# Kernel optimization log

Measured on AMD Instinct MI355X. Metric: run time of the kernel, lower is better.

The kernel has to match this reference:

```python
import jax, jax.numpy as jnp
import numpy as np

DIM = 1024
HEADS = 16
DIM_HEAD = 64
INNER = HEADS * DIM_HEAD  # 1024
EPS = 1e-5


def _layernorm(x, gamma, beta):
    mu = jnp.mean(x, axis=-1, keepdims=True)
    var = jnp.var(x, axis=-1, keepdims=True)
    return (x - mu) * jax.lax.rsqrt(var + EPS) * gamma + beta


def setup_inputs() -> dict:
    key = jax.random.key(0)
    ks = jax.random.split(key, 7)
    b, m, n = 8, 4096, 64
    x = jax.random.normal(ks[0], (b, m, DIM), dtype=jnp.float32)
    latents = jax.random.normal(ks[1], (b, n, DIM), dtype=jnp.float32)
    # LayerNorm params (torch default: weight=1, bias=0; randomize slightly)
    g1 = jnp.ones((DIM,), jnp.float32)
    b1 = jnp.zeros((DIM,), jnp.float32)
    g2 = jnp.ones((DIM,), jnp.float32)
    b2 = jnp.zeros((DIM,), jnp.float32)
    s = 1.0 / np.sqrt(DIM)
    Wq = jax.random.normal(ks[2], (DIM, INNER), jnp.float32) * s   # [in, out]
    Wkv = jax.random.normal(ks[3], (DIM, 2 * INNER), jnp.float32) * s
    Wo = jax.random.normal(ks[4], (INNER, DIM), jnp.float32) * s
    return {"x": x, "latents": latents, "g1": g1, "b1": b1,
            "g2": g2, "b2": b2, "Wq": Wq, "Wkv": Wkv, "Wo": Wo}


def reference(x, latents, g1, b1, g2, b2, Wq, Wkv, Wo):
    b, n, _ = latents.shape
    h, d = HEADS, DIM_HEAD
    scale = d ** -0.5

    xn = _layernorm(x, g1, b1)
    ln = _layernorm(latents, g2, b2)

    q = ln @ Wq                              # [b, n, inner]
    kv_input = jnp.concatenate((xn, ln), axis=1)  # [b, m+n, dim]
    kv = kv_input @ Wkv                      # [b, m+n, 2*inner]
    k, v = jnp.split(kv, 2, axis=-1)
    s_kv = kv_input.shape[1]

    q = q.reshape(b, n, h, d).transpose(0, 2, 1, 3)      # bhnd
    k = k.reshape(b, s_kv, h, d).transpose(0, 2, 1, 3)   # bhsd
    v = v.reshape(b, s_kv, h, d).transpose(0, 2, 1, 3)   # bhsd

    # double-scaling trick: (q*scale) @ (k*scale)^T  => effective 1/d
    weight = jnp.einsum('bhnd,bhsd->bhns', q * scale, k * scale)
    weight = jax.nn.softmax(weight.astype(jnp.float32), axis=-1).astype(weight.dtype)
    out = jnp.einsum('bhns,bhsd->bhnd', weight, v)
    out = out.transpose(0, 2, 1, 3).reshape(b, n, h * d)
    return out @ Wo
```

## Files before the change

### kernel.cpp

```cpp
#include <hip/hip_runtime.h>

typedef __bf16 bf16;
typedef bf16 bf16x4_t __attribute__((ext_vector_type(4)));
typedef bf16 bf16x8_t __attribute__((ext_vector_type(8)));
typedef float f32x4_t __attribute__((ext_vector_type(4)));

#define DI __device__ __forceinline__

DI void gload_lds16(const void* g, void* l) {
  __builtin_amdgcn_global_load_lds((const __attribute__((address_space(1))) void*)g,
                                   (__attribute__((address_space(3))) void*)l, 16, 0, 0);
}

DI f32x4_t mfma16(bf16x8_t a, bf16x8_t b, f32x4_t c) {
  return __builtin_amdgcn_mfma_f32_16x16x32_bf16(a, b, c, 0, 0, 0);
}

DI unsigned short bfbits(float f) {
  bf16 h = (bf16)f;
  return __builtin_bit_cast(unsigned short, h);
}

__global__ __launch_bounds__(256) void ln_all(const float* __restrict__ x,
                                              const float* __restrict__ lat,
                                              const float* __restrict__ g1,
                                              const float* __restrict__ b1,
                                              const float* __restrict__ g2,
                                              const float* __restrict__ b2,
                                              bf16* __restrict__ kv_in,
                                              bf16* __restrict__ lnq) {
  const int row = blockIdx.x;
  const int t = threadIdx.x;
  const float* in;
  const float* gamma;
  const float* beta;
  size_t orow;
  bool dual;
  int lrow = 0;
  if (row < 32768) {
    in = x + (size_t)row * 1024;
    gamma = g1; beta = b1;
    const int b = row >> 12, r2 = row & 4095;
    orow = (size_t)b * 4160 + r2;
    dual = false;
  } else {
    const int r = row - 32768;
    in = lat + (size_t)r * 1024;
    gamma = g2; beta = b2;
    const int b = r >> 6, r2 = r & 63;
    orow = (size_t)b * 4160 + 4096 + r2;
    dual = true;
    lrow = r;
  }
  const float4 v = ((const float4*)in)[t];
  float s = v.x + v.y + v.z + v.w;
  float q = v.x * v.x + v.y * v.y + v.z * v.z + v.w * v.w;
#pragma unroll
  for (int off = 1; off < 64; off <<= 1) {
    s += __shfl_xor(s, off);
    q += __shfl_xor(q, off);
  }
  __shared__ float red[8];
  const int w = t >> 6;
  if ((t & 63) == 0) { red[w] = s; red[w + 4] = q; }
  __syncthreads();
  s = red[0] + red[1] + red[2] + red[3];
  q = red[4] + red[5] + red[6] + red[7];
  const float mu = s * (1.f / 1024.f);
  const float var = q * (1.f / 1024.f) - mu * mu;
  const float rs = rsqrtf(var + 1e-5f);
  const float4 gv = ((const float4*)gamma)[t];
  const float4 bv = ((const float4*)beta)[t];
  bf16x4_t o;
  o[0] = (bf16)((v.x - mu) * rs * gv.x + bv.x);
  o[1] = (bf16)((v.y - mu) * rs * gv.y + bv.y);
  o[2] = (bf16)((v.z - mu) * rs * gv.z + bv.z);
  o[3] = (bf16)((v.w - mu) * rs * gv.w + bv.w);
  *(bf16x4_t*)(kv_in + orow * 1024 + t * 4) = o;
  if (dual) {
    *(bf16x4_t*)(lnq + (size_t)lrow * 1024 + t * 4) = o;
  }
}

__global__ __launch_bounds__(256) void transpose_all(const float* __restrict__ Wq,
                                                     const float* __restrict__ Wkv,
                                                     const float* __restrict__ Wo,
                                                     bf16* __restrict__ Wq_t,
                                                     bf16* __restrict__ Wkv_t,
                                                     bf16* __restrict__ Wo_t) {
  __shared__ float tile[32][33];
  const int bid = blockIdx.x;
  const float* W;
  bf16* Wt;
  int C, t0;
  if (bid < 1024)      { W = Wq;  Wt = Wq_t;  C = 1024; t0 = bid; }
  else if (bid < 3072) { W = Wkv; Wt = Wkv_t; C = 2048; t0 = bid - 1024; }
  else                 { W = Wo;  Wt = Wo_t;  C = 1024; t0 = bid - 3072; }
  const int R = 1024;
  const int ntx = C >> 5;
  const int c0 = (t0 % ntx) * 32, r0 = (t0 / ntx) * 32;
  const int tx = threadIdx.x, ty = threadIdx.y;
#pragma unroll
  for (int j = 0; j < 4; ++j)
    tile[ty + j * 8][tx] = W[(size_t)(r0 + ty + j * 8) * C + c0 + tx];
  __syncthreads();
#pragma unroll
  for (int j = 0; j < 4; ++j)
    Wt[(size_t)(c0 + ty + j * 8) * R + r0 + tx] = (bf16)tile[tx][ty + j * 8];
}

__global__ __launch_bounds__(256) void gemm_bt(const bf16* __restrict__ A,
                                               const bf16* __restrict__ Bt,
                                               float* __restrict__ Cf,
                                               int M, int N, int K) {
  __shared__ bf16 As[128 * 32];
  __shared__ bf16 Bs[128 * 32];
  const int tid = threadIdx.x;
  const int w = tid >> 6, l = tid & 63;
  const int lg = l >> 4, lr = l & 15;
  const int m0 = blockIdx.y * 128, n0 = blockIdx.x * 128;
  const int wm = w >> 1, wn = w & 1;

  f32x4_t acc[4][4];
#pragma unroll
  for (int i = 0; i < 4; ++i)
#pragma unroll
    for (int j = 0; j < 4; ++j)
      acc[i][j] = f32x4_t{0.f, 0.f, 0.f, 0.f};

  const int nk = K >> 5;
  for (int kt = 0; kt < nk; ++kt) {
    const int k0 = kt * 32;
#pragma unroll
    for (int j = 0; j < 2; ++j) {
      const int rb = j * 64 + w * 16;
      const int r = rb + (l >> 2);
      const int c = (l & 3) * 8;
      gload_lds16(A + (size_t)(m0 + r) * K + k0 + c, &As[rb * 32]);
      gload_lds16(Bt + (size_t)(n0 + r) * K + k0 + c, &Bs[rb * 32]);
    }
    __syncthreads();
    bf16x8_t af[4], bfr[4];
#pragma unroll
    for (int i = 0; i < 4; ++i) {
      af[i] = *(const bf16x8_t*)&As[(wm * 64 + i * 16 + lr) * 32 + lg * 8];
      bfr[i] = *(const bf16x8_t*)&Bs[(wn * 64 + i * 16 + lr) * 32 + lg * 8];
    }
#pragma unroll
    for (int mf = 0; mf < 4; ++mf)
#pragma unroll
      for (int nf = 0; nf < 4; ++nf)
        acc[mf][nf] = mfma16(af[mf], bfr[nf], acc[mf][nf]);
    __syncthreads();
  }

#pragma unroll
  for (int mf = 0; mf < 4; ++mf)
#pragma unroll
    for (int r = 0; r < 4; ++r) {
      const int grow = m0 + wm * 64 + mf * 16 + 4 * lg + r;
#pragma unroll
      for (int nf = 0; nf < 4; ++nf) {
        const int gcol = n0 + wn * 64 + nf * 16 + lr;
        Cf[(size_t)grow * N + gcol] = acc[mf][nf][r];
      }
    }
}

__global__ __launch_bounds__(512, 2) void gemm256_kv(const bf16* __restrict__ Akv,
                                                     const bf16* __restrict__ Aq,
                                                     const bf16* __restrict__ BtKV,
                                                     const bf16* __restrict__ BtQ,
                                                     bf16* __restrict__ Kout,
                                                     bf16* __restrict__ Vout,
                                                     bf16* __restrict__ Qout) {
  extern __shared__ char lds[];
  const int tid = threadIdx.x;
  const int w = tid >> 6, l = tid & 63;
  const int lr = l & 15, lg = l >> 4;
  const int wr = w >> 2, wc = w & 3;

  const int cpx = gridDim.x >> 3;
  const int swz = (blockIdx.x & 7) * cpx + (blockIdx.x >> 3);
  const bool isQ = swz >= 1040;
  const bf16* Ap;
  const bf16* Bp;
  int m0, n0;
  if (!isQ) {
    m0 = (swz >> 3) << 8;
    n0 = (swz & 7) << 8;
    Ap = Akv; Bp = BtKV;
  } else {
    const int qi = swz - 1040;
    m0 = (qi >> 2) << 8;
    n0 = (qi & 3) << 8;
    Ap = Aq; Bp = BtQ;
  }

  auto stage = [&](const bf16* __restrict__ G, int row0, int k0, char* base, int half) {
#pragma unroll
    for (int j = 0; j < 2; ++j) {
      const int r0 = half * 128 + (w * 2 + j) * 8;
      const int row = r0 + (l >> 3);
      const int col = ((l & 7) ^ (l >> 3)) * 8;
      gload_lds16(G + (size_t)(row0 + row) * 1024 + k0 + col, base + r0 * 128);
    }
  };
  auto rdA = [&](char* base, int mf, int ks) -> bf16x8_t {
    const int row = wr * 128 + mf * 16 + lr;
    int byte = row * 128 + (ks * 32 + lg * 8) * 2;
    byte ^= (row & 7) << 4;
    return *(const bf16x8_t*)(base + byte);
  };
  auto rdB = [&](char* base, int nf, int ks) -> bf16x8_t {
    const int row = wc * 64 + nf * 16 + lr;
    int byte = row * 128 + (ks * 32 + lg * 8) * 2;
    byte ^= (row & 7) << 4;
    return *(const bf16x8_t*)(base + byte);
  };

  f32x4_t acc[8][4];
#pragma unroll
  for (int i = 0; i < 8; ++i)
#pragma unroll
    for (int j = 0; j < 4; ++j)
      acc[i][j] = f32x4_t{0.f, 0.f, 0.f, 0.f};

  const int NK = 16;

  stage(Ap, m0, 0, lds, 0);
  stage(Ap, m0, 0, lds, 1);
  stage(Bp, n0, 0, lds + 32768, 0);
  stage(Bp, n0, 0, lds + 32768, 1);
  stage(Ap, m0, 64, lds + 65536, 0);
  stage(Ap, m0, 64, lds + 65536, 1);
  asm volatile("s_waitcnt vmcnt(4)" ::: "memory");
  __builtin_amdgcn_s_barrier();

  bf16x8_t ra[4][2], rb[4][2];
  for (int kt = 0; kt < NK; ++kt) {
    const int cur = kt & 1, nxt = cur ^ 1;
    char* Ac = lds + cur * 65536;
    char* Bc = lds + 32768 + cur * 65536;
    char* Bn = lds + 32768 + nxt * 65536;
    const int k1 = (kt + 1) << 6, k2 = (kt + 2) << 6;

#pragma unroll
    for (int mf = 0; mf < 4; ++mf) { ra[mf][0] = rdA(Ac, mf, 0); ra[mf][1] = rdA(Ac, mf, 1); }
#pragma unroll
    for (int nf = 0; nf < 2; ++nf) { rb[nf][0] = rdB(Bc, nf, 0); rb[nf][1] = rdB(Bc, nf, 1); }
    if (kt + 1 < NK) stage(Bp, n0, k1, Bn, 0);
    asm volatile("s_waitcnt lgkmcnt(0)" ::: "memory");
    __builtin_amdgcn_sched_barrier(0);
    __builtin_amdgcn_s_barrier();
    __builtin_amdgcn_s_setprio(1);
#pragma unroll
    for (int mf = 0; mf < 4; ++mf)
#pragma unroll
      for (int nf = 0; nf < 2; ++nf) {
        acc[mf][nf] = mfma16(ra[mf][0], rb[nf][0], acc[mf][nf]);
        acc[mf][nf] = mfma16(ra[mf][1], rb[nf][1], acc[mf][nf]);
      }
    __builtin_amdgcn_s_setprio(0);

#pragma unroll
    for (int nf = 2; nf < 4; ++nf) { rb[nf][0] = rdB(Bc, nf, 0); rb[nf][1] = rdB(Bc, nf, 1); }
    if (kt + 1 < NK) stage(Bp, n0, k1, Bn, 1);
    asm volatile("s_waitcnt lgkmcnt(0)" ::: "memory");
    __builtin_amdgcn_sched_barrier(0);
    __builtin_amdgcn_s_barrier();
    __builtin_amdgcn_s_setprio(1);
#pragma unroll
    for (int mf = 0; mf < 4; ++mf)
#pragma unroll
      for (int nf = 2; nf < 4; ++nf) {
        acc[mf][nf] = mfma16(ra[mf][0], rb[nf][0], acc[mf][nf]);
        acc[mf][nf] = mfma16(ra[mf][1], rb[nf][1], acc[mf][nf]);
      }
    __builtin_amdgcn_s_setprio(0);

#pragma unroll
    for (int mf = 0; mf < 4; ++mf) { ra[mf][0] = rdA(Ac, mf + 4, 0); ra[mf][1] = rdA(Ac, mf + 4, 1); }
    asm volatile("s_waitcnt lgkmcnt(0)" ::: "memory");
    __builtin_amdgcn_sched_barrier(0);
    __builtin_amdgcn_s_barrier();
    __builtin_amdgcn_s_setprio(1);
#pragma unroll
    for (int mf = 0; mf < 4; ++mf)
#pragma unroll
      for (int nf = 0; nf < 2; ++nf) {
        acc[mf + 4][nf] = mfma16(ra[mf][0], rb[nf][0], acc[mf + 4][nf]);
        acc[mf + 4][nf] = mfma16(ra[mf][1], rb[nf][1], acc[mf + 4][nf]);
      }
    __builtin_amdgcn_s_setprio(0);

    if (kt + 2 < NK) { stage(Ap, m0, k2, Ac, 0); stage(Ap, m0, k2, Ac, 1); }
    if (kt + 2 < NK)
      asm volatile("s_waitcnt vmcnt(4)" ::: "memory");
    else
      asm volatile("s_waitcnt vmcnt(0)" ::: "memory");
    __builtin_amdgcn_sched_barrier(0);
    __builtin_amdgcn_s_barrier();
    __builtin_amdgcn_s_setprio(1);
#pragma unroll
    for (int mf = 0; mf < 4; ++mf)
#pragma unroll
      for (int nf = 2; nf < 4; ++nf) {
        acc[mf + 4][nf] = mfma16(ra[mf][0], rb[nf][0], acc[mf + 4][nf]);
        acc[mf + 4][nf] = mfma16(ra[mf][1], rb[nf][1], acc[mf + 4][nf]);
      }
    __builtin_amdgcn_s_setprio(0);
  }

  if (isQ) {
#pragma unroll
    for (int mf = 0; mf < 8; ++mf) {
      const int grow0 = m0 + wr * 128 + mf * 16 + 4 * lg;
#pragma unroll
      for (int nf = 0; nf < 4; ++nf) {
        const int gcol = n0 + wc * 64 + nf * 16 + lr;
        const int h = gcol >> 6, d = gcol & 63;
#pragma unroll
        for (int r = 0; r < 4; ++r) {
          const int grow = grow0 + r;
          const int b = grow >> 6, i = grow & 63;
          Qout[((size_t)((b * 16 + h) * 64 + i)) * 64 + d] = (bf16)acc[mf][nf][r];
        }
      }
    }
    return;
  }
#pragma unroll
  for (int mf = 0; mf < 8; ++mf) {
    const int grow0 = m0 + wr * 128 + mf * 16 + 4 * lg;
#pragma unroll
    for (int nf = 0; nf < 4; ++nf) {
      const int gcol = n0 + wc * 64 + nf * 16 + lr;
      if (gcol < 1024) {
        const int h = gcol >> 6, d = gcol & 63;
#pragma unroll
        for (int r = 0; r < 4; ++r) {
          const int grow = grow0 + r;
          const int bb = grow / 4160, s = grow % 4160;
          Kout[((size_t)((bb * 16 + h) * 4160 + s)) * 64 + d] = (bf16)acc[mf][nf][r];
        }
      } else {
        const int c2 = gcol - 1024, h = c2 >> 6, d = c2 & 63;
        const int bb = grow0 / 4160, s0 = grow0 % 4160;
        ushort4 u;
        u.x = bfbits(acc[mf][nf][0]);
        u.y = bfbits(acc[mf][nf][1]);
        u.z = bfbits(acc[mf][nf][2]);
        u.w = bfbits(acc[mf][nf][3]);
        *(ushort4*)&Vout[((size_t)((bb * 16 + h) * 64 + d)) * 4160 + s0] = u;
      }
    }
  }
}

__global__ __launch_bounds__(256) void attn_part(const bf16* __restrict__ qb_,
                                                 const bf16* __restrict__ kb_,
                                                 const bf16* __restrict__ vb_,
                                                 float* __restrict__ ob,
                                                 float* __restrict__ mb,
                                                 float* __restrict__ lb) {
  const int c = blockIdx.x;
  const int bh = blockIdx.y;
  const int tid = threadIdx.x;
  const int wave = tid >> 6, l = tid & 63;
  const int lg = l >> 4, lr = l & 15;
  const int qr0 = wave * 16;

  const bf16* q = qb_ + ((size_t)bh * 64 + qr0) * 64;
  const bf16* Kp = kb_ + (size_t)bh * 4160 * 64;
  const bf16* Vt = vb_ + (size_t)bh * 64 * 4160;

  bf16x8_t qf[2];
#pragma unroll
  for (int kk = 0; kk < 2; ++kk)
    qf[kk] = *(const bf16x8_t*)(q + lr * 64 + kk * 32 + lg * 8);

  f32x4_t oacc[4];
  float m[4], lsum[4];
#pragma unroll
  for (int r = 0; r < 4; ++r) { m[r] = -1e30f; lsum[r] = 0.f; }
#pragma unroll
  for (int nf = 0; nf < 4; ++nf) oacc[nf] = f32x4_t{0.f, 0.f, 0.f, 0.f};

  __shared__ bf16 plds[4][16][72];
  bf16(*P)[72] = plds[wave];

  constexpr float inv = 1.0f / 64.0f;

  for (int kt = 0; kt < 13; ++kt) {
    const int key0 = c * 832 + kt * 64;
    f32x4_t sf[4];
#pragma unroll
    for (int nf = 0; nf < 4; ++nf) sf[nf] = f32x4_t{0.f, 0.f, 0.f, 0.f};
#pragma unroll
    for (int kk = 0; kk < 2; ++kk)
#pragma unroll
      for (int nf = 0; nf < 4; ++nf) {
        bf16x8_t kf = *(const bf16x8_t*)(Kp + (size_t)(key0 + nf * 16 + lr) * 64 + kk * 32 + lg * 8);
        sf[nf] = mfma16(qf[kk], kf, sf[nf]);
      }
    float corr[4];
#pragma unroll
    for (int r = 0; r < 4; ++r) {
      float t = fmaxf(fmaxf(sf[0][r], sf[1][r]), fmaxf(sf[2][r], sf[3][r])) * inv;
#pragma unroll
      for (int off = 1; off < 16; off <<= 1) t = fmaxf(t, __shfl_xor(t, off));
      const float mn = fmaxf(t, m[r]);
      corr[r] = __expf(m[r] - mn);
      m[r] = mn;
    }
    float rowsum[4] = {0.f, 0.f, 0.f, 0.f};
#pragma unroll
    for (int nf = 0; nf < 4; ++nf)
#pragma unroll
      for (int r = 0; r < 4; ++r) {
        const float p = __expf(sf[nf][r] * inv - m[r]);
        rowsum[r] += p;
        P[lg * 4 + r][nf * 16 + lr] = (bf16)p;
      }
#pragma unroll
    for (int r = 0; r < 4; ++r) {
      float t = rowsum[r];
#pragma unroll
      for (int off = 1; off < 16; off <<= 1) t += __shfl_xor(t, off);
      lsum[r] = lsum[r] * corr[r] + t;
    }
#pragma unroll
    for (int nf = 0; nf < 4; ++nf) {
      oacc[nf][0] *= corr[0];
      oacc[nf][1] *= corr[1];
      oacc[nf][2] *= corr[2];
      oacc[nf][3] *= corr[3];
    }
    asm volatile("s_waitcnt lgkmcnt(0)" ::: "memory");
#pragma unroll
    for (int kk = 0; kk < 2; ++kk) {
      bf16x8_t pf = *(const bf16x8_t*)&P[lr][kk * 32 + lg * 8];
#pragma unroll
      for (int nf = 0; nf < 4; ++nf) {
        bf16x8_t vf = *(const bf16x8_t*)(Vt + (size_t)(nf * 16 + lr) * 4160 + key0 + kk * 32 + lg * 8);
        oacc[nf] = mfma16(pf, vf, oacc[nf]);
      }
    }
    asm volatile("s_waitcnt lgkmcnt(0)" ::: "memory");
  }

#pragma unroll
  for (int nf = 0; nf < 4; ++nf)
#pragma unroll
    for (int r = 0; r < 4; ++r) {
      const int i = qr0 + lg * 4 + r;
      ob[((size_t)((bh * 64 + i) * 5 + c)) * 64 + nf * 16 + lr] = oacc[nf][r];
    }
  if (lr == 0) {
#pragma unroll
    for (int r = 0; r < 4; ++r) {
      const int i = qr0 + lg * 4 + r;
      mb[(bh * 64 + i) * 5 + c] = m[r];
      lb[(bh * 64 + i) * 5 + c] = lsum[r];
    }
  }
}

__global__ __launch_bounds__(256) void attn_merge(const float* __restrict__ ob,
                                                  const float* __restrict__ mb,
                                                  const float* __restrict__ lb,
                                                  bf16* __restrict__ aout) {
  const int j = blockIdx.x * 4 + (threadIdx.x >> 6);
  const int l = threadIdx.x & 63;
  float mv[5];
  float mx = -1e30f;
#pragma unroll
  for (int cc = 0; cc < 5; ++cc) { mv[cc] = mb[j * 5 + cc]; mx = fmaxf(mx, mv[cc]); }
  float L = 0.f, o = 0.f;
#pragma unroll
  for (int cc = 0; cc < 5; ++cc) {
    const float wgt = __expf(mv[cc] - mx);
    L += lb[j * 5 + cc] * wgt;
    o += wgt * ob[((size_t)(j * 5 + cc)) * 64 + l];
  }
  const int bh = j >> 6, i = j & 63, b = bh >> 4, h = bh & 15;
  aout[((size_t)(b * 64 + i)) * 1024 + h * 64 + l] = (bf16)(o / L);
}

extern "C" void kernel_launch(void* const* d_in, const int* in_sizes, int n_in,
                              void* d_out, int out_size, void* d_ws, size_t ws_size,
                              hipStream_t stream) {
  (void)in_sizes; (void)n_in; (void)out_size; (void)ws_size;
  const float* x   = (const float*)d_in[0];
  const float* lat = (const float*)d_in[1];
  const float* g1  = (const float*)d_in[2];
  const float* b1  = (const float*)d_in[3];
  const float* g2  = (const float*)d_in[4];
  const float* b2  = (const float*)d_in[5];
  const float* Wq  = (const float*)d_in[6];
  const float* Wkv = (const float*)d_in[7];
  const float* Wo  = (const float*)d_in[8];
  float* out = (float*)d_out;

  char* ws = (char*)d_ws;
  size_t off = 0;
  auto alloc = [&](size_t bytes) {
    void* p = ws + off;
    off += (bytes + 255) & ~(size_t)255;
    return p;
  };
  bf16* kv_in = (bf16*)alloc(8ull * 4160 * 1024 * 2);
  bf16* Wkv_t = (bf16*)alloc(2048ull * 1024 * 2);
  bf16* Wq_t  = (bf16*)alloc(1024ull * 1024 * 2);
  bf16* Wo_t  = (bf16*)alloc(1024ull * 1024 * 2);
  bf16* lnq   = (bf16*)alloc(512ull * 1024 * 2);
  bf16* qbuf  = (bf16*)alloc(512ull * 1024 * 2);
  bf16* kbuf  = (bf16*)alloc(8ull * 16 * 4160 * 64 * 2);
  bf16* vtbuf = (bf16*)alloc(8ull * 16 * 4160 * 64 * 2);
  bf16* aout  = (bf16*)alloc(512ull * 1024 * 2);

  float* obuf = (float*)kv_in;
  float* mbuf = obuf + 8192ull * 5 * 64;
  float* lbuf = mbuf + 8192ull * 5;

  (void)hipFuncSetAttribute(reinterpret_cast<const void*>(gemm256_kv),
                            hipFuncAttributeMaxDynamicSharedMemorySize, 131072);

  transpose_all<<<4096, dim3(32, 8), 0, stream>>>(Wq, Wkv, Wo, Wq_t, Wkv_t, Wo_t);
  ln_all<<<33280, 256, 0, stream>>>(x, lat, g1, b1, g2, b2, kv_in, lnq);

  gemm256_kv<<<1048, 512, 131072, stream>>>(kv_in, lnq, Wkv_t, Wq_t, kbuf, vtbuf, qbuf);

  attn_part<<<dim3(5, 128), 256, 0, stream>>>(qbuf, kbuf, vtbuf, obuf, mbuf, lbuf);
  attn_merge<<<2048, 256, 0, stream>>>(obuf, mbuf, lbuf, aout);

  gemm_bt<<<dim3(1024 / 128, 512 / 128), 256, 0, stream>>>(aout, Wo_t, out, 512, 1024, 1024);
}
```

Measured before the change: 304.5 us.

## Fuse layernorm and weight transposes into one prep kernel; prefetch K/V in attention

Merges the weight transpose/cast kernel and the layernorm kernel into a single launch. Layernorm now runs one row per wave with four float4 loads per lane, which removes the shared-memory reduction and the block barrier. The attention partial kernel loads the next K tile into registers while softmax runs on the current one, and issues the V loads before the P-tile wait. This costs more registers in attention and adds branch divergence between block types in the fused prep kernel.

```diff
diff --git a/kernel.cpp b/kernel.cpp
--- a/kernel.cpp
+++ b/kernel.cpp
@@ -21,92 +21,92 @@
   return __builtin_bit_cast(unsigned short, h);
 }
 
-__global__ __launch_bounds__(256) void ln_all(const float* __restrict__ x,
-                                              const float* __restrict__ lat,
-                                              const float* __restrict__ g1,
-                                              const float* __restrict__ b1,
-                                              const float* __restrict__ g2,
-                                              const float* __restrict__ b2,
-                                              bf16* __restrict__ kv_in,
-                                              bf16* __restrict__ lnq) {
-  const int row = blockIdx.x;
+__global__ __launch_bounds__(256) void prep_all(const float* __restrict__ x,
+                                                const float* __restrict__ lat,
+                                                const float* __restrict__ g1,
+                                                const float* __restrict__ b1,
+                                                const float* __restrict__ g2,
+                                                const float* __restrict__ b2,
+                                                const float* __restrict__ Wq,
+                                                const float* __restrict__ Wkv,
+                                                const float* __restrict__ Wo,
+                                                bf16* __restrict__ kv_in,
+                                                bf16* __restrict__ lnq,
+                                                bf16* __restrict__ Wq_t,
+                                                bf16* __restrict__ Wkv_t,
+                                                bf16* __restrict__ Wo_t) {
+  const int bid = blockIdx.x;
   const int t = threadIdx.x;
-  const float* in;
-  const float* gamma;
-  const float* beta;
-  size_t orow;
-  bool dual;
-  int lrow = 0;
-  if (row < 32768) {
-    in = x + (size_t)row * 1024;
-    gamma = g1; beta = b1;
-    const int b = row >> 12, r2 = row & 4095;
-    orow = (size_t)b * 4160 + r2;
-    dual = false;
+  if (bid < 8320) {
+    const int wv = t >> 6, l = t & 63;
+    const int row = bid * 4 + wv;
+    const float* in;
+    const float* gamma;
+    const float* beta;
+    size_t orow;
+    bool dual = false;
+    int lrow = 0;
+    if (row < 32768) {
+      in = x + (size_t)row * 1024;
+      gamma = g1; beta = b1;
+      orow = (size_t)(row >> 12) * 4160 + (row & 4095);
+    } else {
+      const int r = row - 32768;
+      in = lat + (size_t)r * 1024;
+      gamma = g2; beta = b2;
+      orow = (size_t)(r >> 6) * 4160 + 4096 + (r & 63);
+      dual = true;
+      lrow = r;
+    }
+    float4 v[4];
+    float s = 0.f, q = 0.f;
+#pragma unroll
+    for (int i = 0; i < 4; ++i) {
+      v[i] = ((const float4*)in)[i * 64 + l];
+      s += v[i].x + v[i].y + v[i].z + v[i].w;
+      q += v[i].x * v[i].x + v[i].y * v[i].y + v[i].z * v[i].z + v[i].w * v[i].w;
+    }
+#pragma unroll
+    for (int off = 1; off < 64; off <<= 1) {
+      s += __shfl_xor(s, off);
+      q += __shfl_xor(q, off);
+    }
+    const float mu = s * (1.f / 1024.f);
+    const float var = q * (1.f / 1024.f) - mu * mu;
+    const float rs = rsqrtf(var + 1e-5f);
+#pragma unroll
+    for (int i = 0; i < 4; ++i) {
+      const float4 gv = ((const float4*)gamma)[i * 64 + l];
+      const float4 bv = ((const float4*)beta)[i * 64 + l];
+      bf16x4_t o;
+      o[0] = (bf16)((v[i].x - mu) * rs * gv.x + bv.x);
+      o[1] = (bf16)((v[i].y - mu) * rs * gv.y + bv.y);
+      o[2] = (bf16)((v[i].z - mu) * rs * gv.z + bv.z);
+      o[3] = (bf16)((v[i].w - mu) * rs * gv.w + bv.w);
+      *(bf16x4_t*)(kv_in + orow * 1024 + i * 256 + l * 4) = o;
+      if (dual) *(bf16x4_t*)(lnq + (size_t)lrow * 1024 + i * 256 + l * 4) = o;
+    }
   } else {
-    const int r = row - 32768;
-    in = lat + (size_t)r * 1024;
-    gamma = g2; beta = b2;
-    const int b = r >> 6, r2 = r & 63;
-    orow = (size_t)b * 4160 + 4096 + r2;
-    dual = true;
-    lrow = r;
-  }
-  const float4 v = ((const float4*)in)[t];
-  float s = v.x + v.y + v.z + v.w;
-  float q = v.x * v.x + v.y * v.y + v.z * v.z + v.w * v.w;
-#pragma unroll
-  for (int off = 1; off < 64; off <<= 1) {
-    s += __shfl_xor(s, off);
-    q += __shfl_xor(q, off);
-  }
-  __shared__ float red[8];
-  const int w = t >> 6;
-  if ((t & 63) == 0) { red[w] = s; red[w + 4] = q; }
-  __syncthreads();
-  s = red[0] + red[1] + red[2] + red[3];
-  q = red[4] + red[5] + red[6] + red[7];
-  const float mu = s * (1.f / 1024.f);
-  const float var = q * (1.f / 1024.f) - mu * mu;
-  const float rs = rsqrtf(var + 1e-5f);
-  const float4 gv = ((const float4*)gamma)[t];
-  const float4 bv = ((const float4*)beta)[t];
-  bf16x4_t o;
-  o[0] = (bf16)((v.x - mu) * rs * gv.x + bv.x);
-  o[1] = (bf16)((v.y - mu) * rs * gv.y + bv.y);
-  o[2] = (bf16)((v.z - mu) * rs * gv.z + bv.z);
-  o[3] = (bf16)((v.w - mu) * rs * gv.w + bv.w);
-  *(bf16x4_t*)(kv_in + orow * 1024 + t * 4) = o;
-  if (dual) {
-    *(bf16x4_t*)(lnq + (size_t)lrow * 1024 + t * 4) = o;
-  }
-}
-
-__global__ __launch_bounds__(256) void transpose_all(const float* __restrict__ Wq,
-                                                     const float* __restrict__ Wkv,
-                                                     const float* __restrict__ Wo,
-                                                     bf16* __restrict__ Wq_t,
-                                                     bf16* __restrict__ Wkv_t,
-                                                     bf16* __restrict__ Wo_t) {
-  __shared__ float tile[32][33];
-  const int bid = blockIdx.x;
-  const float* W;
-  bf16* Wt;
-  int C, t0;
-  if (bid < 1024)      { W = Wq;  Wt = Wq_t;  C = 1024; t0 = bid; }
-  else if (bid < 3072) { W = Wkv; Wt = Wkv_t; C = 2048; t0 = bid - 1024; }
-  else                 { W = Wo;  Wt = Wo_t;  C = 1024; t0 = bid - 3072; }
-  const int R = 1024;
-  const int ntx = C >> 5;
-  const int c0 = (t0 % ntx) * 32, r0 = (t0 / ntx) * 32;
-  const int tx = threadIdx.x, ty = threadIdx.y;
-#pragma unroll
-  for (int j = 0; j < 4; ++j)
-    tile[ty + j * 8][tx] = W[(size_t)(r0 + ty + j * 8) * C + c0 + tx];
-  __syncthreads();
-#pragma unroll
-  for (int j = 0; j < 4; ++j)
-    Wt[(size_t)(c0 + ty + j * 8) * R + r0 + tx] = (bf16)tile[tx][ty + j * 8];
+    __shared__ float tile[32][33];
+    const int b2i = bid - 8320;
+    const float* W;
+    bf16* Wt;
+    int C, t0;
+    if (b2i < 1024)      { W = Wq;  Wt = Wq_t;  C = 1024; t0 = b2i; }
+    else if (b2i < 3072) { W = Wkv; Wt = Wkv_t; C = 2048; t0 = b2i - 1024; }
+    else                 { W = Wo;  Wt = Wo_t;  C = 1024; t0 = b2i - 3072; }
+    const int R = 1024;
+    const int ntx = C >> 5;
+    const int c0 = (t0 % ntx) * 32, r0 = (t0 / ntx) * 32;
+    const int tx = t & 31, ty = t >> 5;
+#pragma unroll
+    for (int j = 0; j < 4; ++j)
+      tile[ty + j * 8][tx] = W[(size_t)(r0 + ty + j * 8) * C + c0 + tx];
+    __syncthreads();
+#pragma unroll
+    for (int j = 0; j < 4; ++j)
+      Wt[(size_t)(c0 + ty + j * 8) * R + r0 + tx] = (bf16)tile[tx][ty + j * 8];
+  }
 }
 
 __global__ __launch_bounds__(256) void gemm_bt(const bf16* __restrict__ A,
@@ -392,6 +392,16 @@
 
   constexpr float inv = 1.0f / 64.0f;
 
+  bf16x8_t kf[2][4];
+  auto ldK = [&](int key0) {
+#pragma unroll
+    for (int kk = 0; kk < 2; ++kk)
+#pragma unroll
+      for (int nf = 0; nf < 4; ++nf)
+        kf[kk][nf] = *(const bf16x8_t*)(Kp + (size_t)(key0 + nf * 16 + lr) * 64 + kk * 32 + lg * 8);
+  };
+
+  ldK(c * 832);
   for (int kt = 0; kt < 13; ++kt) {
     const int key0 = c * 832 + kt * 64;
     f32x4_t sf[4];
@@ -400,10 +410,9 @@
 #pragma unroll
     for (int kk = 0; kk < 2; ++kk)
 #pragma unroll
-      for (int nf = 0; nf < 4; ++nf) {
-        bf16x8_t kf = *(const bf16x8_t*)(Kp + (size_t)(key0 + nf * 16 + lr) * 64 + kk * 32 + lg * 8);
-        sf[nf] = mfma16(qf[kk], kf, sf[nf]);
-      }
+      for (int nf = 0; nf < 4; ++nf)
+        sf[nf] = mfma16(qf[kk], kf[kk][nf], sf[nf]);
+    if (kt + 1 < 13) ldK(key0 + 64);
     float corr[4];
 #pragma unroll
     for (int r = 0; r < 4; ++r) {
@@ -437,15 +446,19 @@
       oacc[nf][2] *= corr[2];
       oacc[nf][3] *= corr[3];
     }
+    bf16x8_t vf[2][4];
+#pragma unroll
+    for (int kk = 0; kk < 2; ++kk)
+#pragma unroll
+      for (int nf = 0; nf < 4; ++nf)
+        vf[kk][nf] = *(const bf16x8_t*)(Vt + (size_t)(nf * 16 + lr) * 4160 + key0 + kk * 32 + lg * 8);
     asm volatile("s_waitcnt lgkmcnt(0)" ::: "memory");
 #pragma unroll
     for (int kk = 0; kk < 2; ++kk) {
       bf16x8_t pf = *(const bf16x8_t*)&P[lr][kk * 32 + lg * 8];
 #pragma unroll
-      for (int nf = 0; nf < 4; ++nf) {
-        bf16x8_t vf = *(const bf16x8_t*)(Vt + (size_t)(nf * 16 + lr) * 4160 + key0 + kk * 32 + lg * 8);
-        oacc[nf] = mfma16(pf, vf, oacc[nf]);
-      }
+      for (int nf = 0; nf < 4; ++nf)
+        oacc[nf] = mfma16(pf, vf[kk][nf], oacc[nf]);
     }
     asm volatile("s_waitcnt lgkmcnt(0)" ::: "memory");
   }
@@ -527,8 +540,8 @@
   (void)hipFuncSetAttribute(reinterpret_cast<const void*>(gemm256_kv),
                             hipFuncAttributeMaxDynamicSharedMemorySize, 131072);
 
-  transpose_all<<<4096, dim3(32, 8), 0, stream>>>(Wq, Wkv, Wo, Wq_t, Wkv_t, Wo_t);
-  ln_all<<<33280, 256, 0, stream>>>(x, lat, g1, b1, g2, b2, kv_in, lnq);
+  prep_all<<<12416, 256, 0, stream>>>(x, lat, g1, b1, g2, b2, Wq, Wkv, Wo,
+                                      kv_in, lnq, Wq_t, Wkv_t, Wo_t);
 
   gemm256_kv<<<1048, 512, 131072, stream>>>(kv_in, lnq, Wkv_t, Wq_t, kbuf, vtbuf, qbuf);
 
```

Result: faster. 291.4 us (-4.3%).
